# Kernel tuning notes

Measured on AMD Instinct MI355X. Metric: run time of the kernel, lower is better.

## Reference

```python
import jax, jax.numpy as jnp
import numpy as np

DIM = 512
HEADS = 8
HEAD_DIM = DIM // HEADS
EPS = 1e-5

def _ln(x, g, b):
    m = jnp.mean(x, axis=-1, keepdims=True)
    v = jnp.mean((x - m) ** 2, axis=-1, keepdims=True)
    return (x - m) * jax.lax.rsqrt(v + EPS) * g + b

def setup_inputs() -> dict:
    key = jax.random.key(0)
    ks = jax.random.split(key, 12)
    s = 0.02
    d, dff = DIM, 4 * DIM
    inp = {
        'x': jax.random.normal(ks[0], (8, 4096, d), jnp.float32),
        'Wq': jax.random.normal(ks[1], (d, d), jnp.float32) * s,
        'bq': jnp.zeros((d,), jnp.float32),
        'Wk': jax.random.normal(ks[2], (d, d), jnp.float32) * s,
        'bk': jnp.zeros((d,), jnp.float32),
        'Wv': jax.random.normal(ks[3], (d, d), jnp.float32) * s,
        'bv': jnp.zeros((d,), jnp.float32),
        'Wo': jax.random.normal(ks[4], (d, d), jnp.float32) * s,
        'bo': jnp.zeros((d,), jnp.float32),
        'g1': jnp.ones((d,), jnp.float32),
        'b1': jnp.zeros((d,), jnp.float32),
        'g2': jnp.ones((d,), jnp.float32),
        'b2': jnp.zeros((d,), jnp.float32),
        'Wf1': jax.random.normal(ks[5], (d, dff), jnp.float32) * s,
        'bf1': jnp.zeros((dff,), jnp.float32),
        'Wf2': jax.random.normal(ks[6], (dff, d), jnp.float32) * s,
        'bf2': jnp.zeros((d,), jnp.float32),
    }
    return inp

def _linear_attn(x, Wq, bq, Wk, bk, Wv, bv, Wo, bo):
    b, n, d = x.shape
    def split(t):
        return t.reshape(b, n, HEADS, HEAD_DIM).transpose(0, 2, 1, 3)  # bhnd
    q = split(x @ Wq + bq)
    k = split(x @ Wk + bk)
    v = split(x @ Wv + bv)
    q = jax.nn.elu(q) + 1.0
    k = jax.nn.elu(k) + 1.0
    kv = jnp.einsum('bhnd,bhnf->bhdf', k, v)
    out = jnp.einsum('bhnd,bhdf->bhnf', q, kv)
    out = out.transpose(0, 2, 1, 3).reshape(b, n, d)
    return out @ Wo + bo

def reference(x, Wq, bq, Wk, bk, Wv, bv, Wo, bo, g1, b1, g2, b2, Wf1, bf1, Wf2, bf2):
    # series decomposition: AvgPool1d(k=3, stride=1, pad=1, count_include_pad=True)
    xp = jnp.pad(x, ((0, 0), (1, 1), (0, 0)))
    trend = (xp[:, :-2] + xp[:, 1:-1] + xp[:, 2:]) / 3.0
    seasonal = x - trend
    seasonal = seasonal + _linear_attn(_ln(seasonal, g1, b1), Wq, bq, Wk, bk, Wv, bv, Wo, bo)
    h = _ln(seasonal, g2, b2)
    h = jax.nn.gelu(h @ Wf1 + bf1, approximate=False) @ Wf2 + bf2
    seasonal = seasonal + h
    return seasonal + trend
```

## Files before the change

### kernel.cpp

```cpp
#include <hip/hip_runtime.h>
#include <math.h>

typedef __bf16 bf16;
typedef __attribute__((ext_vector_type(8))) __bf16 bf16x8;
typedef __attribute__((ext_vector_type(4))) float floatx4;

#define DIM 512
#define DFF 2048
#define SEQ 4096
#define ROWS 32768

#define GLOBAL_AS(p) ((const __attribute__((address_space(1))) void*)(p))
#define LDS_AS(p)    ((__attribute__((address_space(3))) void*)(p))

__global__ __launch_bounds__(256) void prep_w_kernel(const float* __restrict__ W,
                                                     bf16* __restrict__ Wt, int K, int N)
{
    int idx = blockIdx.x * 256 + threadIdx.x;
    if (idx >= K * N) return;
    int k = idx % K;
    int n = idx / K;
    Wt[idx] = (bf16)W[(size_t)k * N + n];
}

__global__ __launch_bounds__(256) void pack_bias_kernel(const float* __restrict__ bq,
                                                        const float* __restrict__ bk,
                                                        const float* __restrict__ bv,
                                                        float* __restrict__ out)
{
    int i = blockIdx.x * 256 + threadIdx.x;
    if (i >= 1536) return;
    out[i] = (i < 512) ? bq[i] : (i < 1024 ? bk[i - 512] : bv[i - 1024]);
}

__device__ inline float wave_red(float v)
{
#pragma unroll
    for (int off = 32; off; off >>= 1) v += __shfl_xor(v, off, 64);
    return v;
}

__global__ __launch_bounds__(256) void decomp_ln_kernel(const float* __restrict__ x,
                                                        const float* __restrict__ g,
                                                        const float* __restrict__ be,
                                                        float* __restrict__ S,
                                                        bf16* __restrict__ XN)
{
    int wave = threadIdx.x >> 6, lane = threadIdx.x & 63;
    int r = blockIdx.x * 4 + wave;
    int n = r & (SEQ - 1);
    const float4* xr = (const float4*)(x + (size_t)r * DIM);
    float4 z = make_float4(0.f, 0.f, 0.f, 0.f);
    float s[8];
#pragma unroll
    for (int i = 0; i < 2; ++i) {
        int c4 = lane * 2 + i;
        float4 v0 = xr[c4];
        float4 vm = (n > 0)       ? xr[c4 - DIM / 4] : z;
        float4 vp = (n < SEQ - 1) ? xr[c4 + DIM / 4] : z;
        s[i * 4 + 0] = v0.x - (vm.x + v0.x + vp.x) * (1.f / 3.f);
        s[i * 4 + 1] = v0.y - (vm.y + v0.y + vp.y) * (1.f / 3.f);
        s[i * 4 + 2] = v0.z - (vm.z + v0.z + vp.z) * (1.f / 3.f);
        s[i * 4 + 3] = v0.w - (vm.w + v0.w + vp.w) * (1.f / 3.f);
    }
    float4* Sr = (float4*)(S + (size_t)r * DIM);
    Sr[lane * 2]     = make_float4(s[0], s[1], s[2], s[3]);
    Sr[lane * 2 + 1] = make_float4(s[4], s[5], s[6], s[7]);

    float sum = 0.f;
#pragma unroll
    for (int j = 0; j < 8; ++j) sum += s[j];
    sum = wave_red(sum);
    float mean = sum * (1.f / DIM);
    float vs = 0.f;
#pragma unroll
    for (int j = 0; j < 8; ++j) { float d = s[j] - mean; vs += d * d; }
    vs = wave_red(vs);
    float rstd = rsqrtf(vs * (1.f / DIM) + 1e-5f);

    int c = lane * 8;
    float4 g0 = ((const float4*)(g + c))[0],  g1v = ((const float4*)(g + c))[1];
    float4 b0 = ((const float4*)(be + c))[0], b1v = ((const float4*)(be + c))[1];
    bf16x8 o;
    o[0] = (bf16)((s[0] - mean) * rstd * g0.x + b0.x);
    o[1] = (bf16)((s[1] - mean) * rstd * g0.y + b0.y);
    o[2] = (bf16)((s[2] - mean) * rstd * g0.z + b0.z);
    o[3] = (bf16)((s[3] - mean) * rstd * g0.w + b0.w);
    o[4] = (bf16)((s[4] - mean) * rstd * g1v.x + b1v.x);
    o[5] = (bf16)((s[5] - mean) * rstd * g1v.y + b1v.y);
    o[6] = (bf16)((s[6] - mean) * rstd * g1v.z + b1v.z);
    o[7] = (bf16)((s[7] - mean) * rstd * g1v.w + b1v.w);
    *(bf16x8*)(XN + (size_t)r * DIM + c) = o;
}

__global__ __launch_bounds__(256) void ln_kernel(const float* __restrict__ X,
                                                 const float* __restrict__ g,
                                                 const float* __restrict__ be,
                                                 bf16* __restrict__ XN)
{
    int wave = threadIdx.x >> 6, lane = threadIdx.x & 63;
    int r = blockIdx.x * 4 + wave;
    const float4* xr = (const float4*)(X + (size_t)r * DIM);
    float4 a0 = xr[lane * 2], a1 = xr[lane * 2 + 1];
    float s[8] = {a0.x, a0.y, a0.z, a0.w, a1.x, a1.y, a1.z, a1.w};
    float sum = 0.f;
#pragma unroll
    for (int j = 0; j < 8; ++j) sum += s[j];
    sum = wave_red(sum);
    float mean = sum * (1.f / DIM);
    float vs = 0.f;
#pragma unroll
    for (int j = 0; j < 8; ++j) { float d = s[j] - mean; vs += d * d; }
    vs = wave_red(vs);
    float rstd = rsqrtf(vs * (1.f / DIM) + 1e-5f);
    int c = lane * 8;
    float4 g0 = ((const float4*)(g + c))[0],  g1v = ((const float4*)(g + c))[1];
    float4 b0 = ((const float4*)(be + c))[0], b1v = ((const float4*)(be + c))[1];
    bf16x8 o;
    o[0] = (bf16)((s[0] - mean) * rstd * g0.x + b0.x);
    o[1] = (bf16)((s[1] - mean) * rstd * g0.y + b0.y);
    o[2] = (bf16)((s[2] - mean) * rstd * g0.z + b0.z);
    o[3] = (bf16)((s[3] - mean) * rstd * g0.w + b0.w);
    o[4] = (bf16)((s[4] - mean) * rstd * g1v.x + b1v.x);
    o[5] = (bf16)((s[5] - mean) * rstd * g1v.y + b1v.y);
    o[6] = (bf16)((s[6] - mean) * rstd * g1v.z + b1v.z);
    o[7] = (bf16)((s[7] - mean) * rstd * g1v.w + b1v.w);
    *(bf16x8*)(XN + (size_t)r * DIM + c) = o;
}

enum { M_QKV = 0, M_ATTN = 1, M_FFN1 = 2, M_FFN2 = 3 };

template <int MODE>
__global__ __launch_bounds__(256) void gemm_bt_kernel(const bf16* __restrict__ A, int lda,
                                                      const bf16* __restrict__ Bt,
                                                      const float* __restrict__ bias,
                                                      float* S, const float* __restrict__ X,
                                                      void* Cout, int ldc,
                                                      int N, int K, int rows_per_batch,
                                                      int m_off)
{
    __shared__ __align__(16) bf16 lA[128 * 32];
    __shared__ __align__(16) bf16 lB[128 * 32];
    int tid = threadIdx.x;
    int m0 = blockIdx.y * 128;
    int n0 = blockIdx.x * 128;
    const bf16* Abase = A + (size_t)m0 * lda;
    const bf16* Bbase = Bt + (size_t)n0 * K;
    if (rows_per_batch) Bbase += (size_t)(m0 / rows_per_batch) * (size_t)N * K;

    int lane = tid & 63;
    int wave = tid >> 6;
    int wm = (wave >> 1) * 64;
    int wn = (wave & 1) * 64;
    int lm = lane & 15;
    int quad = lane >> 4;
    int i0w = tid & 192;

    floatx4 acc[4][4];
#pragma unroll
    for (int i = 0; i < 4; ++i)
#pragma unroll
        for (int j = 0; j < 4; ++j) acc[i][j] = (floatx4){0.f, 0.f, 0.f, 0.f};

    for (int k0 = 0; k0 < K; k0 += 32) {
        __syncthreads();
#pragma unroll
        for (int it = 0; it < 2; ++it) {
            int ib = it * 256 + i0w;
            int i  = ib + lane;
            int row = i >> 2;
            int col = (i & 3) * 8;
            __builtin_amdgcn_global_load_lds(GLOBAL_AS(Abase + (size_t)row * lda + k0 + col),
                                             LDS_AS(&lA[ib * 8]), 16, 0, 0);
            __builtin_amdgcn_global_load_lds(GLOBAL_AS(Bbase + (size_t)row * K + k0 + col),
                                             LDS_AS(&lB[ib * 8]), 16, 0, 0);
        }
        __syncthreads();

        bf16x8 af[4], bfv[4];
#pragma unroll
        for (int i = 0; i < 4; ++i)
            af[i] = *(const bf16x8*)&lA[(wm + i * 16 + lm) * 32 + quad * 8];
#pragma unroll
        for (int j = 0; j < 4; ++j)
            bfv[j] = *(const bf16x8*)&lB[(wn + j * 16 + lm) * 32 + quad * 8];
#pragma unroll
        for (int i = 0; i < 4; ++i)
#pragma unroll
            for (int j = 0; j < 4; ++j)
                acc[i][j] = __builtin_amdgcn_mfma_f32_16x16x32_bf16(af[i], bfv[j], acc[i][j], 0, 0, 0);
    }

#pragma unroll
    for (int i = 0; i < 4; ++i) {
        int gm_base = m0 + wm + i * 16 + quad * 4;
#pragma unroll
        for (int j = 0; j < 4; ++j) {
            int gn = n0 + wn + j * 16 + lm;
            float bia = bias[gn];
#pragma unroll
            for (int e = 0; e < 4; ++e) {
                int gm = gm_base + e;
                float val = acc[i][j][e] + bia;
                if constexpr (MODE == M_QKV) {
                    if (gn < 1024) val = (val > 0.f) ? val + 1.f : __expf(val);
                    ((bf16*)Cout)[(size_t)gm * ldc + gn] = (bf16)val;
                } else if constexpr (MODE == M_ATTN) {
                    S[(size_t)gm * DIM + gn] += val;
                } else if constexpr (MODE == M_FFN1) {
                    val = 0.5f * val * (1.f + erff(val * 0.70710678118654752f));
                    ((bf16*)Cout)[(size_t)gm * ldc + gn] = (bf16)val;
                } else {
                    int gmg = m_off + gm;
                    int nn = gmg & (SEQ - 1);
                    size_t o = (size_t)gmg * DIM + gn;
                    float xc = X[o];
                    float xm = (nn > 0)       ? X[o - DIM] : 0.f;
                    float xp = (nn < SEQ - 1) ? X[o + DIM] : 0.f;
                    float* op = (float*)Cout;
                    op[o] = val + op[o] + (xm + xc + xp) * (1.f / 3.f);
                }
            }
        }
    }
}

__global__ __launch_bounds__(256) void kv_mfma_kernel(const bf16* __restrict__ QKV,
                                                      float* __restrict__ KV)
{
    int kc = blockIdx.x, h = blockIdx.y, b = blockIdx.z;
    __shared__ __align__(16) bf16 lbuf[2 * 128 * 64];
    bf16* lk = lbuf;
    bf16* lv = lbuf + 128 * 64;
    int tid = threadIdx.x;
    int lane = tid & 63, wave = tid >> 6;
    int lm = lane & 15, quad = lane >> 4;

    floatx4 acc[4][4];
#pragma unroll
    for (int i = 0; i < 4; ++i)
#pragma unroll
        for (int j = 0; j < 4; ++j) acc[i][j] = (floatx4){0.f, 0.f, 0.f, 0.f};

    const bf16* kb = QKV + (size_t)b * SEQ * 1536 + 512 + (size_t)h * 64;
    const bf16* vb = kb + 512;
    int drow = lane >> 3;
    int d0 = (lane & 7) * 8;

    for (int it = 0; it < 8; ++it) {
        int n0 = kc * 1024 + it * 128;
        __syncthreads();
#pragma unroll
        for (int q = 0; q < 4; ++q) {
            int nbase = wave * 32 + q * 8;
            int ldsoff = wave * 2048 + q * 512;
            __builtin_amdgcn_global_load_lds(GLOBAL_AS(kb + (size_t)(n0 + nbase + drow) * 1536 + d0),
                                             LDS_AS(&lk[ldsoff]), 16, 0, 0);
            __builtin_amdgcn_global_load_lds(GLOBAL_AS(vb + (size_t)(n0 + nbase + drow) * 1536 + d0),
                                             LDS_AS(&lv[ldsoff]), 16, 0, 0);
        }
        __syncthreads();

        int nw = wave * 32 + quad * 8;
        bf16x8 af[4], bfv[4];
#pragma unroll
        for (int i = 0; i < 4; ++i) {
            int dd = i * 16 + lm;
#pragma unroll
            for (int j = 0; j < 8; ++j) af[i][j] = lk[(nw + j) * 64 + dd];
#pragma unroll
            for (int j = 0; j < 8; ++j) bfv[i][j] = lv[(nw + j) * 64 + dd];
        }
#pragma unroll
        for (int i = 0; i < 4; ++i)
#pragma unroll
            for (int j = 0; j < 4; ++j)
                acc[i][j] = __builtin_amdgcn_mfma_f32_16x16x32_bf16(af[i], bfv[j], acc[i][j], 0, 0, 0);
    }

    __syncthreads();
    float* red = (float*)lbuf;
    if (wave < 2) {
#pragma unroll
        for (int i = 0; i < 4; ++i)
#pragma unroll
            for (int j = 0; j < 4; ++j)
#pragma unroll
                for (int e = 0; e < 4; ++e)
                    red[wave * 4096 + (i * 16 + quad * 4 + e) * 64 + j * 16 + lm] = acc[i][j][e];
    }
    __syncthreads();
    if (wave >= 2) {
#pragma unroll
        for (int i = 0; i < 4; ++i)
#pragma unroll
            for (int j = 0; j < 4; ++j)
#pragma unroll
                for (int e = 0; e < 4; ++e)
                    red[(wave - 2) * 4096 + (i * 16 + quad * 4 + e) * 64 + j * 16 + lm] += acc[i][j][e];
    }
    __syncthreads();
    float* dst = KV + ((size_t)kc * 64 + b * 8 + h) * 4096;
#pragma unroll
    for (int p = 0; p < 4; ++p) {
        int e4 = (tid + p * 256) * 4;
        float4 a = *(const float4*)&red[e4];
        float4 c4 = *(const float4*)&red[4096 + e4];
        a.x += c4.x; a.y += c4.y; a.z += c4.z; a.w += c4.w;
        *(float4*)&dst[e4] = a;
    }
}

__global__ __launch_bounds__(256) void kvw_kernel(const float* __restrict__ KV,
                                                  const float* __restrict__ Wo,
                                                  bf16* __restrict__ KVWT)
{
    int jc = blockIdx.x & 7, bh = blockIdx.x >> 3;
    int h = bh & 7, b = bh >> 3;
    __shared__ float skvT[64 * 68];
    int tid = threadIdx.x;
    const float* src = KV + (size_t)bh * 4096;
#pragma unroll
    for (int p = 0; p < 16; ++p) {
        int e = tid + p * 256;
        float s = src[e] + src[e + 262144] + src[e + 524288] + src[e + 786432];
        skvT[(e & 63) * 68 + (e >> 6)] = s;
    }
    __syncthreads();

    int j = tid & 63, dq = tid >> 6;
    int j0 = jc * 64;
    floatx4 acc4[4];
#pragma unroll
    for (int c = 0; c < 4; ++c) acc4[c] = (floatx4){0.f, 0.f, 0.f, 0.f};
    const float* wop = Wo + (size_t)h * 64 * 512 + j0 + j;
#pragma unroll 8
    for (int f = 0; f < 64; ++f) {
        float w = wop[(size_t)f * 512];
        const float* sp = &skvT[f * 68 + dq * 16];
#pragma unroll
        for (int c = 0; c < 4; ++c) {
            floatx4 s = *(const floatx4*)(sp + c * 4);
            acc4[c] += s * w;
        }
    }
    bf16* dst = KVWT + (size_t)b * 262144 + (size_t)(j0 + j) * 512 + h * 64 + dq * 16;
    bf16x8 o0, o1;
#pragma unroll
    for (int t = 0; t < 8; ++t) { o0[t] = (bf16)acc4[t >> 2][t & 3]; o1[t] = (bf16)acc4[2 + (t >> 2)][t & 3]; }
    *(bf16x8*)dst = o0;
    *(bf16x8*)(dst + 8) = o1;
}

extern "C" void kernel_launch(void* const* d_in, const int* in_sizes, int n_in,
                              void* d_out, int out_size, void* d_ws, size_t ws_size,
                              hipStream_t stream)
{
    const float* x   = (const float*)d_in[0];
    const float* Wq  = (const float*)d_in[1];
    const float* bq  = (const float*)d_in[2];
    const float* Wk  = (const float*)d_in[3];
    const float* bk  = (const float*)d_in[4];
    const float* Wv  = (const float*)d_in[5];
    const float* bv  = (const float*)d_in[6];
    const float* Wo  = (const float*)d_in[7];
    const float* bo  = (const float*)d_in[8];
    const float* g1  = (const float*)d_in[9];
    const float* b1  = (const float*)d_in[10];
    const float* g2  = (const float*)d_in[11];
    const float* b2  = (const float*)d_in[12];
    const float* Wf1 = (const float*)d_in[13];
    const float* bf1 = (const float*)d_in[14];
    const float* Wf2 = (const float*)d_in[15];
    const float* bf2 = (const float*)d_in[16];
    float* out = (float*)d_out;
    (void)in_sizes; (void)n_in; (void)out_size; (void)ws_size;

    char* ws = (char*)d_ws;
    size_t off = 0;
    auto alloc = [&](size_t bytes) -> char* {
        char* p = ws + off;
        off += (bytes + 255) & ~(size_t)255;
        return p;
    };
    bf16*  WqkvT = (bf16*)alloc((size_t)1536 * 512 * 2);
    float* bias3 = (float*)alloc(1536 * 4);
    bf16*  Wf1T  = (bf16*)alloc((size_t)2048 * 512 * 2);
    bf16*  Wf2T  = (bf16*)alloc((size_t)512 * 2048 * 2);
    bf16*  XN    = (bf16*)alloc((size_t)ROWS * DIM * 2);
    float* KV    = (float*)alloc((size_t)4 * 64 * 4096 * 4);
    bf16*  KVWT  = (bf16*)alloc((size_t)8 * 512 * 512 * 2);
    bf16*  QKV   = (bf16*)alloc((size_t)ROWS * 1536 * 2);
    bf16*  H1    = QKV;

    prep_w_kernel<<<1024, 256, 0, stream>>>(Wq, WqkvT,              512, 512);
    prep_w_kernel<<<1024, 256, 0, stream>>>(Wk, WqkvT + 512 * 512,  512, 512);
    prep_w_kernel<<<1024, 256, 0, stream>>>(Wv, WqkvT + 1024 * 512, 512, 512);
    prep_w_kernel<<<4096, 256, 0, stream>>>(Wf1, Wf1T, 512, 2048);
    prep_w_kernel<<<4096, 256, 0, stream>>>(Wf2, Wf2T, 2048, 512);
    pack_bias_kernel<<<6, 256, 0, stream>>>(bq, bk, bv, bias3);

    decomp_ln_kernel<<<8192, 256, 0, stream>>>(x, g1, b1, out, XN);

    gemm_bt_kernel<M_QKV><<<dim3(12, 256), 256, 0, stream>>>(
        XN, 512, WqkvT, bias3, nullptr, nullptr, QKV, 1536, 1536, 512, 0, 0);

    kv_mfma_kernel<<<dim3(4, 8, 8), 256, 0, stream>>>(QKV, KV);

    kvw_kernel<<<512, 256, 0, stream>>>(KV, Wo, KVWT);

    gemm_bt_kernel<M_ATTN><<<dim3(4, 256), 256, 0, stream>>>(
        QKV, 1536, KVWT, bo, out, nullptr, nullptr, 0, 512, 512, 4096, 0);

    ln_kernel<<<8192, 256, 0, stream>>>(out, g2, b2, XN);

    for (int c = 0; c < 2; ++c) {
        gemm_bt_kernel<M_FFN1><<<dim3(16, 128), 256, 0, stream>>>(
            XN + (size_t)c * 16384 * 512, 512, Wf1T, bf1, nullptr, nullptr,
            H1, 2048, 2048, 512, 0, 0);
        gemm_bt_kernel<M_FFN2><<<dim3(4, 128), 256, 0, stream>>>(
            H1, 2048, Wf2T, bf2, nullptr, x, out, 512, 512, 2048, 0, c * 16384);
    }
}
```

Baseline: 725.0 us.

## Swizzle GEMM LDS layout, move trend add into LN, single FFN chunk

Applies an XOR swizzle to the K-column placement in the GEMM LDS tiles so that fragment reads avoid bank conflicts. The trend (3-tap average of x) is now added to the residual inside the second LayerNorm kernel instead of in the FFN2 epilogue, so FFN2 becomes a plain accumulate GEMM. When the workspace is large enough, the full FFN hidden buffer is allocated so FFN1/FFN2 run as one chunk instead of two. This removes scattered neighbour-row loads from the GEMM epilogue and some launch and tail overhead, at the cost of an extra read-modify-write pass over S in the LN kernel and more workspace memory.

```diff
diff --git a/kernel.cpp b/kernel.cpp
--- a/kernel.cpp
+++ b/kernel.cpp
@@ -93,15 +93,17 @@
     *(bf16x8*)(XN + (size_t)r * DIM + c) = o;
 }
 
-__global__ __launch_bounds__(256) void ln_kernel(const float* __restrict__ X,
-                                                 const float* __restrict__ g,
-                                                 const float* __restrict__ be,
-                                                 bf16* __restrict__ XN)
+__global__ __launch_bounds__(256) void ln_trend_kernel(const float* __restrict__ x,
+                                                       const float* __restrict__ g,
+                                                       const float* __restrict__ be,
+                                                       float* __restrict__ S,
+                                                       bf16* __restrict__ XN)
 {
     int wave = threadIdx.x >> 6, lane = threadIdx.x & 63;
     int r = blockIdx.x * 4 + wave;
-    const float4* xr = (const float4*)(X + (size_t)r * DIM);
-    float4 a0 = xr[lane * 2], a1 = xr[lane * 2 + 1];
+    int n = r & (SEQ - 1);
+    float4* Sr = (float4*)(S + (size_t)r * DIM);
+    float4 a0 = Sr[lane * 2], a1 = Sr[lane * 2 + 1];
     float s[8] = {a0.x, a0.y, a0.z, a0.w, a1.x, a1.y, a1.z, a1.w};
     float sum = 0.f;
 #pragma unroll
@@ -126,18 +128,32 @@
     o[6] = (bf16)((s[6] - mean) * rstd * g1v.z + b1v.z);
     o[7] = (bf16)((s[7] - mean) * rstd * g1v.w + b1v.w);
     *(bf16x8*)(XN + (size_t)r * DIM + c) = o;
-}
-
-enum { M_QKV = 0, M_ATTN = 1, M_FFN1 = 2, M_FFN2 = 3 };
+
+    const float4* xr = (const float4*)(x + (size_t)r * DIM);
+    float4 z = make_float4(0.f, 0.f, 0.f, 0.f);
+#pragma unroll
+    for (int i = 0; i < 2; ++i) {
+        int c4 = lane * 2 + i;
+        float4 v0 = xr[c4];
+        float4 vm = (n > 0)       ? xr[c4 - DIM / 4] : z;
+        float4 vp = (n < SEQ - 1) ? xr[c4 + DIM / 4] : z;
+        float4 sv = (i == 0) ? a0 : a1;
+        sv.x += (vm.x + v0.x + vp.x) * (1.f / 3.f);
+        sv.y += (vm.y + v0.y + vp.y) * (1.f / 3.f);
+        sv.z += (vm.z + v0.z + vp.z) * (1.f / 3.f);
+        sv.w += (vm.w + v0.w + vp.w) * (1.f / 3.f);
+        Sr[c4] = sv;
+    }
+}
+
+enum { M_QKV = 0, M_ACC = 1, M_FFN1 = 2 };
 
 template <int MODE>
 __global__ __launch_bounds__(256) void gemm_bt_kernel(const bf16* __restrict__ A, int lda,
                                                       const bf16* __restrict__ Bt,
                                                       const float* __restrict__ bias,
-                                                      float* S, const float* __restrict__ X,
-                                                      void* Cout, int ldc,
-                                                      int N, int K, int rows_per_batch,
-                                                      int m_off)
+                                                      float* S, void* Cout, int ldc,
+                                                      int N, int K, int rows_per_batch)
 {
     __shared__ __align__(16) bf16 lA[128 * 32];
     __shared__ __align__(16) bf16 lB[128 * 32];
@@ -155,6 +171,7 @@
     int lm = lane & 15;
     int quad = lane >> 4;
     int i0w = tid & 192;
+    int swz = (lm >> 1) & 3;
 
     floatx4 acc[4][4];
 #pragma unroll
@@ -169,7 +186,7 @@
             int ib = it * 256 + i0w;
             int i  = ib + lane;
             int row = i >> 2;
-            int col = (i & 3) * 8;
+            int col = ((i & 3) ^ ((row >> 1) & 3)) * 8;
             __builtin_amdgcn_global_load_lds(GLOBAL_AS(Abase + (size_t)row * lda + k0 + col),
                                              LDS_AS(&lA[ib * 8]), 16, 0, 0);
             __builtin_amdgcn_global_load_lds(GLOBAL_AS(Bbase + (size_t)row * K + k0 + col),
@@ -180,10 +197,10 @@
         bf16x8 af[4], bfv[4];
 #pragma unroll
         for (int i = 0; i < 4; ++i)
-            af[i] = *(const bf16x8*)&lA[(wm + i * 16 + lm) * 32 + quad * 8];
+            af[i] = *(const bf16x8*)&lA[(wm + i * 16 + lm) * 32 + (quad ^ swz) * 8];
 #pragma unroll
         for (int j = 0; j < 4; ++j)
-            bfv[j] = *(const bf16x8*)&lB[(wn + j * 16 + lm) * 32 + quad * 8];
+            bfv[j] = *(const bf16x8*)&lB[(wn + j * 16 + lm) * 32 + (quad ^ swz) * 8];
 #pragma unroll
         for (int i = 0; i < 4; ++i)
 #pragma unroll
@@ -205,20 +222,11 @@
                 if constexpr (MODE == M_QKV) {
                     if (gn < 1024) val = (val > 0.f) ? val + 1.f : __expf(val);
                     ((bf16*)Cout)[(size_t)gm * ldc + gn] = (bf16)val;
-                } else if constexpr (MODE == M_ATTN) {
+                } else if constexpr (MODE == M_ACC) {
                     S[(size_t)gm * DIM + gn] += val;
-                } else if constexpr (MODE == M_FFN1) {
+                } else {
                     val = 0.5f * val * (1.f + erff(val * 0.70710678118654752f));
                     ((bf16*)Cout)[(size_t)gm * ldc + gn] = (bf16)val;
-                } else {
-                    int gmg = m_off + gm;
-                    int nn = gmg & (SEQ - 1);
-                    size_t o = (size_t)gmg * DIM + gn;
-                    float xc = X[o];
-                    float xm = (nn > 0)       ? X[o - DIM] : 0.f;
-                    float xp = (nn < SEQ - 1) ? X[o + DIM] : 0.f;
-                    float* op = (float*)Cout;
-                    op[o] = val + op[o] + (xm + xc + xp) * (1.f / 3.f);
                 }
             }
         }
@@ -374,7 +382,7 @@
     const float* Wf2 = (const float*)d_in[15];
     const float* bf2 = (const float*)d_in[16];
     float* out = (float*)d_out;
-    (void)in_sizes; (void)n_in; (void)out_size; (void)ws_size;
+    (void)in_sizes; (void)n_in; (void)out_size;
 
     char* ws = (char*)d_ws;
     size_t off = 0;
@@ -391,7 +399,12 @@
     float* KV    = (float*)alloc((size_t)4 * 64 * 4096 * 4);
     bf16*  KVWT  = (bf16*)alloc((size_t)8 * 512 * 512 * 2);
     bf16*  QKV   = (bf16*)alloc((size_t)ROWS * 1536 * 2);
-    bf16*  H1    = QKV;
+    size_t base_need = off;
+    size_t h1_full = (size_t)ROWS * DFF * 2;
+    bool big = (ws_size >= base_need + h1_full);
+    bf16* H1 = big ? (bf16*)alloc(h1_full) : QKV;
+    int n_chunks   = big ? 1 : 2;
+    int chunk_rows = big ? ROWS : ROWS / 2;
 
     prep_w_kernel<<<1024, 256, 0, stream>>>(Wq, WqkvT,              512, 512);
     prep_w_kernel<<<1024, 256, 0, stream>>>(Wk, WqkvT + 512 * 512,  512, 512);
@@ -403,22 +416,23 @@
     decomp_ln_kernel<<<8192, 256, 0, stream>>>(x, g1, b1, out, XN);
 
     gemm_bt_kernel<M_QKV><<<dim3(12, 256), 256, 0, stream>>>(
-        XN, 512, WqkvT, bias3, nullptr, nullptr, QKV, 1536, 1536, 512, 0, 0);
+        XN, 512, WqkvT, bias3, nullptr, QKV, 1536, 1536, 512, 0);
 
     kv_mfma_kernel<<<dim3(4, 8, 8), 256, 0, stream>>>(QKV, KV);
 
     kvw_kernel<<<512, 256, 0, stream>>>(KV, Wo, KVWT);
 
-    gemm_bt_kernel<M_ATTN><<<dim3(4, 256), 256, 0, stream>>>(
-        QKV, 1536, KVWT, bo, out, nullptr, nullptr, 0, 512, 512, 4096, 0);
-
-    ln_kernel<<<8192, 256, 0, stream>>>(out, g2, b2, XN);
-
-    for (int c = 0; c < 2; ++c) {
-        gemm_bt_kernel<M_FFN1><<<dim3(16, 128), 256, 0, stream>>>(
-            XN + (size_t)c * 16384 * 512, 512, Wf1T, bf1, nullptr, nullptr,
-            H1, 2048, 2048, 512, 0, 0);
-        gemm_bt_kernel<M_FFN2><<<dim3(4, 128), 256, 0, stream>>>(
-            H1, 2048, Wf2T, bf2, nullptr, x, out, 512, 512, 2048, 0, c * 16384);
-    }
-}
+    gemm_bt_kernel<M_ACC><<<dim3(4, 256), 256, 0, stream>>>(
+        QKV, 1536, KVWT, bo, out, nullptr, 0, 512, 512, 4096);
+
+    ln_trend_kernel<<<8192, 256, 0, stream>>>(x, g2, b2, out, XN);
+
+    for (int c = 0; c < n_chunks; ++c) {
+        gemm_bt_kernel<M_FFN1><<<dim3(16, chunk_rows / 128), 256, 0, stream>>>(
+            XN + (size_t)c * chunk_rows * 512, 512, Wf1T, bf1, nullptr,
+            H1, 2048, 2048, 512, 0);
+        gemm_bt_kernel<M_ACC><<<dim3(4, chunk_rows / 128), 256, 0, stream>>>(
+            H1, 2048, Wf2T, bf2, out + (size_t)c * chunk_rows * 512, nullptr,
+            0, 512, 2048, 0);
+    }
+}
```

After: 728.2 us. About the same (+0.4%).
